# Performance work log

Measured on AMD Instinct MI355X. Metric: run time of the kernel, lower is better.

The kernel has to match this reference:

```python
import jax, jax.numpy as jnp
import numpy as np
from jax import lax

MAX_T = 1.0
MAX_Z = float(np.e)  # exp(MAX_T)
BITS = 8


def weight_quantization(w):
    # tanh -> scale by max-abs (no grad through alpha) -> clamp -> round with STE
    w = jnp.tanh(w)
    alpha = lax.stop_gradient(jnp.max(jnp.abs(w)))
    q = 2 ** (BITS - 1) - 1
    w = jnp.clip(w / alpha, -1.0, 1.0) * q
    w = w + lax.stop_gradient(jnp.round(w) - w)
    return w * alpha / q


def t_linear_c(inp, W, max_spike_time):
    # inp: [B, L, Fin], W: [Fout, Fin] -> out: [B, L, Fout]
    idx = jnp.argsort(inp, axis=-1)                              # [B,L,Fin]
    s_inp = jnp.take_along_axis(inp, idx, axis=-1)[..., None]    # [B,L,Fin,1]
    w_sorted = W.T[idx]                                          # [B,L,Fin,Fout]
    w_sorted = weight_quantization(w_sorted)
    mul = s_inp * w_sorted
    w_sum = jnp.cumsum(w_sorted, axis=-2)
    iw_sum = jnp.cumsum(mul, axis=-2)
    out_all = iw_sum / jnp.clip(w_sum - 1.0, 1e-10, 1e10)
    o = jnp.where(w_sum < 1.0, max_spike_time, out_all)
    o = jnp.where(o < s_inp, max_spike_time, o)
    nxt = jnp.concatenate([s_inp[:, :, 1:, :], jnp.ones_like(s_inp[:, :, :1, :])], axis=2)
    o = jnp.where(o > nxt, max_spike_time, o)
    return jnp.min(o, axis=-2)


def t_linear(inp, W, max_spike_time):
    # inp: [B, Fin], W: [Fout, Fin] -> out: [B, Fout]
    idx = jnp.argsort(inp, axis=-1)
    s_inp = jnp.take_along_axis(inp, idx, axis=-1)[..., None]    # [B,Fin,1]
    w_sorted = W.T[idx]                                          # [B,Fin,Fout]
    mul = s_inp * w_sorted
    w_sum = jnp.cumsum(w_sorted, axis=1)
    iw_sum = jnp.cumsum(mul, axis=1)
    out_all = iw_sum / jnp.clip(w_sum - 1.0, 1e-10, 1e10)
    o = jnp.where(w_sum < 1.0, max_spike_time, out_all)
    o = jnp.where(o < s_inp, max_spike_time, o)
    nxt = jnp.concatenate([s_inp[:, 1:, :], jnp.ones_like(s_inp[:, :1, :])], axis=1)
    o = jnp.where(o >= nxt, max_spike_time, o)  # note: >= in t_Linear (vs > in t_Linear_c)
    return jnp.min(o, axis=1)


def unfold(x, k, p, s):
    # torch F.unfold: zero-pad, extract kxk patches; feature order (C, kh, kw)
    B, C, H, W = x.shape
    xp = jnp.pad(x, ((0, 0), (0, 0), (p, p), (p, p)))
    oh = (H + 2 * p - k) // s + 1
    ow = (W + 2 * p - k) // s + 1
    ri = (jnp.arange(oh) * s)[:, None] + jnp.arange(k)           # [oh,k]
    ci = (jnp.arange(ow) * s)[:, None] + jnp.arange(k)           # [ow,k]
    pt = xp[:, :, ri[:, None, :, None], ci[None, :, None, :]]    # [B,C,oh,ow,k,k]
    pt = pt.transpose(0, 2, 3, 1, 4, 5).reshape(B, oh * ow, C * k * k)
    return pt, oh, ow


def t_conv(x, W, k, pad, stride, max_spike_time):
    B = x.shape[0]
    patches, oh, ow = unfold(x, k, pad, stride)                  # [B,L,C*k*k]
    patches = jnp.where(patches < 0.1, max_spike_time, patches)
    out = t_linear_c(patches, W, max_spike_time)                 # [B,L,Cout]
    return out.transpose(0, 2, 1).reshape(B, W.shape[0], oh, ow)


def max_pool2(x):
    return lax.reduce_window(x, -jnp.inf, lax.max, (1, 1, 2, 2), (1, 1, 2, 2), 'VALID')


def min_pool3(x):
    # -MaxPool3x3(stride 2)(-ConstantPad2d(1, 1e5)(x))
    xp = jnp.pad(x, ((0, 0), (0, 0), (1, 1), (1, 1)), constant_values=1e5)
    return -lax.reduce_window(-xp, -jnp.inf, lax.max, (1, 1, 3, 3), (1, 1, 2, 2), 'VALID')


def setup_inputs() -> dict:
    key = jax.random.key(0)
    ks = jax.random.split(key, 8)
    B = 8
    inp = jax.random.normal(ks[0], (B, 1, 64, 64), dtype=jnp.float32)
    conv1_w = jax.random.normal(ks[1], (32, 1, 5, 5), dtype=jnp.float32) * (1.0 / 5.0)
    bn_g = jnp.ones((32,), jnp.float32)
    bn_b = jnp.zeros((32,), jnp.float32)
    bn_m = jnp.zeros((32,), jnp.float32)
    bn_v = jnp.ones((32,), jnp.float32)
    def uw(k, fout, fin):
        return jax.random.uniform(k, (fout, fin), jnp.float32, 0.0, 10.0 / fin)
    w2 = uw(ks[2], 32, 3 * 3 * 32)
    w3 = uw(ks[3], 32, 3 * 3 * 32)
    w4 = uw(ks[4], 64, 3 * 3 * 32)
    w5 = uw(ks[5], 64, 3 * 3 * 64)
    w_fc = uw(ks[6], 10, 8 * 8 * 64)
    return {"inp": inp, "conv1_w": conv1_w, "bn_g": bn_g, "bn_b": bn_b,
            "bn_m": bn_m, "bn_v": bn_v, "w2": w2, "w3": w3, "w4": w4,
            "w5": w5, "w_fc": w_fc}


def reference(inp, conv1_w, bn_g, bn_b, bn_m, bn_v, w2, w3, w4, w5, w_fc):
    x = lax.conv_general_dilated(inp, conv1_w, (1, 1), ((2, 2), (2, 2)),
                                 dimension_numbers=('NCHW', 'OIHW', 'NCHW'))
    x = (x - bn_m[None, :, None, None]) * (bn_g / jnp.sqrt(bn_v + 1e-5))[None, :, None, None] \
        + bn_b[None, :, None, None]
    x = jax.nn.relu(x)
    x = max_pool2(x)                       # [B,32,32,32]
    x = jnp.minimum(x, MAX_T)
    z1 = jnp.exp(x)
    z2 = t_conv(z1, w2, 3, 1, 2, MAX_Z)    # [B,32,16,16]
    z3 = t_conv(z2, w3, 3, 1, 1, MAX_Z)    # [B,32,16,16]
    z3c = z3 * min_pool3(z1)
    z4 = t_conv(z3c, w4, 3, 1, 2, MAX_Z * 2)  # [B,64,8,8]
    z5 = t_conv(z4, w5, 3, 1, 1, MAX_Z * 2)   # [B,64,8,8]
    pm = min_pool3(z3c)                       # [B,32,8,8]
    pm = jnp.concatenate([pm, pm], axis=1)    # [B,64,8,8]
    z5c = (z5 * pm).reshape(z5.shape[0], -1)  # [B,4096]
    return t_linear(z5c, w_fc, MAX_Z * 4)     # [B,10]
```

## Files before the change

### kernel.cpp

```cpp
#include <hip/hip_runtime.h>
#include <hip/hip_bf16.h>
#include <math.h>

#define E32 2.7182817459106445f

__device__ __forceinline__ unsigned long long packkey(float vf, int idx) {
  unsigned u = __float_as_uint(vf);
  u = (u & 0x80000000u) ? ~u : (u | 0x80000000u);
  return (((unsigned long long)u) << 32) | (unsigned)idx;
}
__device__ __forceinline__ float unpackval(unsigned long long k) {
  unsigned m = (unsigned)(k >> 32);
  m = (m & 0x80000000u) ? (m ^ 0x80000000u) : ~m;
  return __uint_as_float(m);
}

__global__ __launch_bounds__(256) void tanh_max_kernel(
    const float* __restrict__ w2, const float* __restrict__ w3,
    const float* __restrict__ w4, const float* __restrict__ w5,
    float* __restrict__ tanhbuf, float* __restrict__ partials) {
  int blk = blockIdx.x;
  const float* w; int base_blk, tbase;
  if (blk < 36)       { w = w2; base_blk = 0;   tbase = 0; }
  else if (blk < 72)  { w = w3; base_blk = 36;  tbase = 9216; }
  else if (blk < 144) { w = w4; base_blk = 72;  tbase = 18432; }
  else                { w = w5; base_blk = 144; tbase = 36864; }
  int i = (blk - base_blk) * 256 + threadIdx.x;
  float t = tanhf(w[i]);
  tanhbuf[tbase + i] = t;
  __shared__ float red[256];
  red[threadIdx.x] = fabsf(t);
  __syncthreads();
  for (int s = 128; s > 0; s >>= 1) {
    if (threadIdx.x < s) red[threadIdx.x] = fmaxf(red[threadIdx.x], red[threadIdx.x + s]);
    __syncthreads();
  }
  if (threadIdx.x == 0) partials[blk] = red[0];
}

__global__ __launch_bounds__(256) void quantT_kernel(
    const float* __restrict__ tanhbuf, const float* __restrict__ partials,
    float* __restrict__ q2, float* __restrict__ q3,
    float* __restrict__ q4, float* __restrict__ q5,
    const float* __restrict__ wfc, float* __restrict__ wfcT) {
  int blk = blockIdx.x;
  if (blk >= 288) {
    int o = (blk - 288) * 256 + threadIdx.x;
    if (o < 40960) {
      int n = o / 10, f = o % 10;
      wfcT[o] = wfc[f * 4096 + n];
    }
    return;
  }
  float* dst; int base_blk, tbase, pb0, pb1, F, N;
  if (blk < 36)       { dst = q2; base_blk = 0;   tbase = 0;     pb0 = 0;   pb1 = 36;  F = 32; N = 288; }
  else if (blk < 72)  { dst = q3; base_blk = 36;  tbase = 9216;  pb0 = 36;  pb1 = 72;  F = 32; N = 288; }
  else if (blk < 144) { dst = q4; base_blk = 72;  tbase = 18432; pb0 = 72;  pb1 = 144; F = 64; N = 288; }
  else                { dst = q5; base_blk = 144; tbase = 36864; pb0 = 144; pb1 = 288; F = 64; N = 576; }
  __shared__ float red[256];
  float mx = 0.0f;
  for (int j = pb0 + threadIdx.x; j < pb1; j += 256) mx = fmaxf(mx, partials[j]);
  red[threadIdx.x] = mx;
  __syncthreads();
  for (int s = 128; s > 0; s >>= 1) {
    if (threadIdx.x < s) red[threadIdx.x] = fmaxf(red[threadIdx.x], red[threadIdx.x + s]);
    __syncthreads();
  }
  float a = red[0];
  int i = (blk - base_blk) * 256 + threadIdx.x;
  float t = tanhbuf[tbase + i];
  int f = i / N, n = i % N;
  float r = fminf(fmaxf(t / a, -1.0f), 1.0f) * 127.0f;
  dst[n * F + f] = rintf(r) * a / 127.0f;
}

__global__ __launch_bounds__(256) void conv1_kernel(
    const float* __restrict__ inp, const float* __restrict__ w,
    const float* __restrict__ g, const float* __restrict__ bb,
    const float* __restrict__ m, const float* __restrict__ vv,
    float* __restrict__ z1) {
  int idx = blockIdx.x * 256 + threadIdx.x;
  if (idx >= 8 * 32 * 32 * 32) return;
  int x = idx & 31, y = (idx >> 5) & 31, c = (idx >> 10) & 31, b = idx >> 15;
  float scale = g[c] / sqrtf(vv[c] + 1e-5f);
  float bias = bb[c];
  float mean = m[c];
  float mx = -3.402823466e38f;
  for (int dy = 0; dy < 2; ++dy) {
    for (int dx = 0; dx < 2; ++dx) {
      int oy = 2 * y + dy, ox = 2 * x + dx;
      float acc = 0.0f;
      for (int kh = 0; kh < 5; ++kh) {
        int r = oy + kh - 2;
        if (r < 0 || r >= 64) continue;
        for (int kw = 0; kw < 5; ++kw) {
          int cc2 = ox + kw - 2;
          if (cc2 < 0 || cc2 >= 64) continue;
          acc += w[c * 25 + kh * 5 + kw] * inp[(b * 64 + r) * 64 + cc2];
        }
      }
      float xs = (acc - mean) * scale + bias;
      xs = fmaxf(xs, 0.0f);
      mx = fmaxf(mx, xs);
    }
  }
  mx = fminf(mx, 1.0f);
  z1[idx] = (mx == 1.0f) ? E32 : expf(mx);
}

__global__ __launch_bounds__(256) void mp3_kernel(
    const float* __restrict__ in, float* __restrict__ out, int BC, int H) {
  int OH = H >> 1;
  int total = BC * OH * OH;
  int idx = blockIdx.x * 256 + threadIdx.x;
  if (idx >= total) return;
  int j = idx % OH, i = (idx / OH) % OH, bc = idx / (OH * OH);
  float mn = 100000.0f;
  for (int di = 0; di < 3; ++di) {
    int r = 2 * i - 1 + di;
    if (r < 0 || r >= H) continue;
    for (int dj = 0; dj < 3; ++dj) {
      int cc = 2 * j - 1 + dj;
      if (cc < 0 || cc >= H) continue;
      mn = fminf(mn, in[bc * H * H + r * H + cc]);
    }
  }
  out[idx] = mn;
}

__global__ __launch_bounds__(256) void mp3mul_kernel(
    const float* __restrict__ a, const float* __restrict__ b2,
    float* __restrict__ out, int BC, int H) {
  int OH = H >> 1;
  int total = BC * OH * OH;
  int idx = blockIdx.x * 256 + threadIdx.x;
  if (idx >= total) return;
  int j = idx % OH, i = (idx / OH) % OH, bc = idx / (OH * OH);
  float mn = 100000.0f;
  for (int di = 0; di < 3; ++di) {
    int r = 2 * i - 1 + di;
    if (r < 0 || r >= H) continue;
    for (int dj = 0; dj < 3; ++dj) {
      int cc = 2 * j - 1 + dj;
      if (cc < 0 || cc >= H) continue;
      int q = bc * H * H + r * H + cc;
      mn = fminf(mn, __fmul_rn(a[q], b2[q]));
    }
  }
  out[idx] = mn;
}

template <int CIN, int F, int S, int HIN, bool MUL>
__global__ __launch_bounds__(512, 1) void tconv_kernel(
    const float* __restrict__ in, const float* __restrict__ in2,
    const float* __restrict__ wqt, float* __restrict__ out, float MST) {
  constexpr int N = CIN * 9;
  constexpr int NP = (N <= 512) ? 512 : 1024;
  constexpr int KP = NP / 512;
  constexpr int OH = (HIN - 1) / S + 1;
  constexpr int P = OH * OH;
  constexpr int T = 512;
  constexpr int NCH = N / 32;

  __shared__ __align__(16) unsigned long long pk[NP];
  __shared__ float sval[N + 1];
  __shared__ unsigned short sidx[N];
  __shared__ float wbuf[2][32 * F];
  __shared__ float wc[NCH][F];
  __shared__ float iwc[NCH][F];
  __shared__ float pmin[F * NCH];

  int blk = blockIdx.x;
  int b = blk / P, p = blk % P;
  int ph = p / OH, pw = p % OH;
  int tid = threadIdx.x;

  for (int n = tid; n < NP; n += T) {
    if (n < N) {
      int c = n / 9, kk = n % 9, kh = kk / 3, kw = kk % 3;
      int r = ph * S + kh - 1, cc = pw * S + kw - 1;
      float v = 0.0f;
      if (r >= 0 && r < HIN && cc >= 0 && cc < HIN) {
        int q = ((b * CIN + c) * HIN + r) * HIN + cc;
        v = MUL ? __fmul_rn(in[q], in2[q]) : in[q];
      }
      pk[n] = packkey((v < 0.1f) ? MST : v, n);
    } else {
      pk[n] = ~0ull;
    }
  }
  if (tid == 0) sval[N] = 1.0f;
  __syncthreads();

  if constexpr (KP == 1) {
    unsigned long long k0 = pk[tid];
    __syncthreads();
    for (int lk = 1; lk <= 9; ++lk) {
      for (int lj = lk - 1; lj >= 0; --lj) {
        int j = 1 << lj;
        bool up = ((tid >> lk) & 1) == 0;
        bool wmin = (((tid & j) == 0) == up);
        unsigned long long o;
        if (lj >= 6) {
          pk[tid] = k0;
          __syncthreads();
          o = pk[tid ^ j];
          __syncthreads();
        } else {
          o = __shfl_xor(k0, j, 64);
        }
        k0 = wmin ? (k0 < o ? k0 : o) : (k0 > o ? k0 : o);
      }
    }
    if (tid < N) {
      sval[tid] = unpackval(k0);
      sidx[tid] = (unsigned short)(k0 & 0xffffull);
    }
  } else {
    unsigned long long k0 = pk[2 * tid], k1 = pk[2 * tid + 1];
    __syncthreads();
    for (int lk = 1; lk <= 10; ++lk) {
      for (int lj = lk - 1; lj >= 0; --lj) {
        bool up = ((tid >> (lk - 1)) & 1) == 0;
        if (lj == 0) {
          if ((k0 > k1) == up) { unsigned long long t2 = k0; k0 = k1; k1 = t2; }
        } else {
          int tj = 1 << (lj - 1);
          bool wmin = (((tid & tj) == 0) == up);
          unsigned long long o0, o1;
          if (lj >= 7) {
            pk[tid] = k0; pk[512 + tid] = k1;
            __syncthreads();
            o0 = pk[tid ^ tj]; o1 = pk[512 + (tid ^ tj)];
            __syncthreads();
          } else {
            o0 = __shfl_xor(k0, tj, 64);
            o1 = __shfl_xor(k1, tj, 64);
          }
          k0 = wmin ? (k0 < o0 ? k0 : o0) : (k0 > o0 ? k0 : o0);
          k1 = wmin ? (k1 < o1 ? k1 : o1) : (k1 > o1 ? k1 : o1);
        }
      }
    }
    int i0 = tid * 2;
    if (i0 < N) {
      sval[i0] = unpackval(k0);
      sidx[i0] = (unsigned short)(k0 & 0xffffull);
    }
    if (i0 + 1 < N) {
      sval[i0 + 1] = unpackval(k1);
      sidx[i0 + 1] = (unsigned short)(k1 & 0xffffull);
    }
  }
  __syncthreads();

  for (int t = tid; t < 32 * F; t += T) {
    int q = t / F, f = t % F;
    wbuf[0][t] = wqt[(int)sidx[q] * F + f];
  }
  __syncthreads();

  float wsum = 0.0f, iwsum = 0.0f;
  for (int c = 0; c < NCH; ++c) {
    if (tid >= 64 && c + 1 < NCH) {
      int i0n = (c + 1) * 32;
      float* nb = wbuf[(c + 1) & 1];
      for (int t = tid - 64; t < 32 * F; t += (T - 64)) {
        int q = t / F, f = t % F;
        nb[t] = wqt[(int)sidx[i0n + q] * F + f];
      }
    }
    if (tid < F) {
      const float* wb = wbuf[c & 1];
      wc[c][tid] = wsum;
      iwc[c][tid] = iwsum;
      int i0 = c * 32;
#pragma unroll
      for (int q0 = 0; q0 < 32; q0 += 8) {
        float w8[8], s8[8];
#pragma unroll
        for (int r = 0; r < 8; ++r) {
          w8[r] = wb[(q0 + r) * F + tid];
          s8[r] = sval[i0 + q0 + r];
        }
#pragma unroll
        for (int r = 0; r < 8; ++r) {
          wsum = __fadd_rn(wsum, w8[r]);
          iwsum = __fadd_rn(iwsum, __fmul_rn(s8[r], w8[r]));
        }
      }
    }
    __syncthreads();
  }

  for (int task = tid; task < NCH * F; task += T) {
    int c = task / F, f = task % F;
    float ws = wc[c][f], iws = iwc[c][f], omin = 3.402823466e38f;
    int i0 = c * 32;
#pragma unroll
    for (int q0 = 0; q0 < 32; q0 += 8) {
      float wv8[8], sv8[8], nv8[8];
#pragma unroll
      for (int r = 0; r < 8; ++r) {
        int i = i0 + q0 + r;
        wv8[r] = wqt[(int)sidx[i] * F + f];
        sv8[r] = sval[i];
        nv8[r] = sval[i + 1];
      }
#pragma unroll
      for (int r = 0; r < 8; ++r) {
        ws = __fadd_rn(ws, wv8[r]);
        iws = __fadd_rn(iws, __fmul_rn(sv8[r], wv8[r]));
        float den = fminf(fmaxf(__fadd_rn(ws, -1.0f), 1e-10f), 1e10f);
        float oa = iws / den;
        float o = (ws < 1.0f) ? MST : oa;
        o = (o < sv8[r]) ? MST : o;
        o = (o > nv8[r]) ? MST : o;
        omin = fminf(omin, o);
      }
    }
    pmin[f * NCH + c] = omin;
  }
  __syncthreads();

  if (tid < F) {
    float m2 = pmin[tid * NCH];
#pragma unroll
    for (int c = 1; c < NCH; ++c) m2 = fminf(m2, pmin[tid * NCH + c]);
    out[(b * F + tid) * P + p] = m2;
  }
}

#define CE(x, y) { int i_ = (tid << 3) + (x); \
  bool up_ = (((i_ >> lk) & 1) == 0); \
  unsigned long long a_ = k[(x)], c_ = k[(y)]; \
  if ((a_ > c_) == up_) { k[(x)] = c_; k[(y)] = a_; } }

__global__ __launch_bounds__(512, 1) void fc_kernel(
    const float* __restrict__ z5, const float* __restrict__ m3,
    const float* __restrict__ wfcT, float* __restrict__ out) {
  constexpr int NN = 4096;
  __shared__ __align__(16) unsigned long long keys[NN];
  __shared__ __align__(16) float sval[NN + 1];
  __shared__ __align__(16) unsigned short sidx[NN];
  __shared__ float wc[64][10];
  __shared__ float iwc[64][10];
  __shared__ float pmin[64][10];
  float* wsA = (float*)keys;
  float* wsB = (float*)keys + 2608;

  int b = blockIdx.x, tid = threadIdx.x, lane = tid & 63;

  unsigned long long k[8];
  {
    int c = tid >> 3, p0 = (tid << 3) & 63;
    const float4* z4p = (const float4*)(z5 + (b * 64 + c) * 64 + p0);
    const float4* m4p = (const float4*)(m3 + (b * 32 + (c & 31)) * 64 + p0);
    float4 za = z4p[0], zb = z4p[1], ma = m4p[0], mb = m4p[1];
    int n0 = tid << 3;
    k[0] = packkey(__fmul_rn(za.x, ma.x), n0 + 0);
    k[1] = packkey(__fmul_rn(za.y, ma.y), n0 + 1);
    k[2] = packkey(__fmul_rn(za.z, ma.z), n0 + 2);
    k[3] = packkey(__fmul_rn(za.w, ma.w), n0 + 3);
    k[4] = packkey(__fmul_rn(zb.x, mb.x), n0 + 4);
    k[5] = packkey(__fmul_rn(zb.y, mb.y), n0 + 5);
    k[6] = packkey(__fmul_rn(zb.z, mb.z), n0 + 6);
    k[7] = packkey(__fmul_rn(zb.w, mb.w), n0 + 7);
  }

  for (int lk = 1; lk <= 12; ++lk) {
    for (int lj = lk - 1; lj >= 0; --lj) {
      if (lj >= 9) {
        int pm = 1 << (lj - 3);
#pragma unroll
        for (int m = 0; m < 8; ++m) keys[m * 512 + tid] = k[m];
        __syncthreads();
        bool lower = ((tid & pm) == 0);
        bool up = (((tid >> (lk - 3)) & 1) == 0);
        bool wmin = (lower == up);
#pragma unroll
        for (int m = 0; m < 8; ++m) {
          unsigned long long o = keys[m * 512 + (tid ^ pm)];
          unsigned long long mine = k[m];
          k[m] = wmin ? (mine < o ? mine : o) : (mine > o ? mine : o);
        }
        __syncthreads();
      } else if (lj >= 3) {
        int lm = 1 << (lj - 3);
        bool lower = ((lane & lm) == 0);
        bool up = (((tid >> (lk - 3)) & 1) == 0);
        bool wmin = (lower == up);
#pragma unroll
        for (int m = 0; m < 8; ++m) {
          unsigned long long o = __shfl_xor(k[m], lm, 64);
          unsigned long long mine = k[m];
          k[m] = wmin ? (mine < o ? mine : o) : (mine > o ? mine : o);
        }
      } else if (lj == 2) {
        CE(0, 4) CE(1, 5) CE(2, 6) CE(3, 7)
      } else if (lj == 1) {
        CE(0, 2) CE(1, 3) CE(4, 6) CE(5, 7)
      } else {
        CE(0, 1) CE(2, 3) CE(4, 5) CE(6, 7)
      }
    }
  }

  {
    float4 v0, v1;
    v0.x = unpackval(k[0]); v0.y = unpackval(k[1]);
    v0.z = unpackval(k[2]); v0.w = unpackval(k[3]);
    v1.x = unpackval(k[4]); v1.y = unpackval(k[5]);
    v1.z = unpackval(k[6]); v1.w = unpackval(k[7]);
    ((float4*)sval)[tid * 2] = v0;
    ((float4*)sval)[tid * 2 + 1] = v1;
    ushort si[8];
#pragma unroll
    for (int m = 0; m < 8; ++m) si[m] = (unsigned short)(k[m] & 0xffffull);
    ((ulong2*)sidx)[tid] = *(ulong2*)si;
  }
  if (tid == 0) sval[NN] = 1.0f;
  __syncthreads();

  {
    float tmp[5];
#pragma unroll
    for (int u = 0; u < 5; ++u) {
      int t = tid + u * 512;
      tmp[u] = wfcT[(int)sidx[t / 10] * 10 + (t % 10)];
    }
#pragma unroll
    for (int u = 0; u < 5; ++u) {
      int t = tid + u * 512;
      wsA[(t % 10) * 260 + t / 10] = tmp[u];
    }
  }
  __syncthreads();

  float wsum = 0.0f, iwsum = 0.0f;
  for (int c = 0; c < 16; ++c) {
    int c0 = c * 256;
    float* cur = (c & 1) ? wsB : wsA;
    float* nxt = (c & 1) ? wsA : wsB;
    if (tid >= 64 && c + 1 < 16) {
      int c0n = c0 + 256;
      float tmp[6];
#pragma unroll
      for (int u = 0; u < 6; ++u) {
        int t = (tid - 64) + u * 448;
        tmp[u] = (t < 2560) ? wfcT[(int)sidx[c0n + t / 10] * 10 + (t % 10)] : 0.0f;
      }
#pragma unroll
      for (int u = 0; u < 6; ++u) {
        int t = (tid - 64) + u * 448;
        if (t < 2560) nxt[(t % 10) * 260 + t / 10] = tmp[u];
      }
    }
    if (tid < 10) {
      const float* wrow = cur + tid * 260;
      float4 wA4[4], sA4[4], wB4[4], sB4[4];
      auto LD = [&](int i0, float4* w4, float4* s4) {
#pragma unroll
        for (int kq = 0; kq < 4; ++kq) {
          w4[kq] = *(const float4*)(wrow + i0 + 4 * kq);
          s4[kq] = *(const float4*)(sval + c0 + i0 + 4 * kq);
        }
      };
      auto ACC = [&](const float4* w4, const float4* s4) {
#pragma unroll
        for (int kq = 0; kq < 4; ++kq) {
          float w0 = w4[kq].x, w1 = w4[kq].y, w2 = w4[kq].z, w3 = w4[kq].w;
          float s0 = s4[kq].x, s1 = s4[kq].y, s2 = s4[kq].z, s3 = s4[kq].w;
          wsum = __fadd_rn(wsum, w0); iwsum = __fadd_rn(iwsum, __fmul_rn(s0, w0));
          wsum = __fadd_rn(wsum, w1); iwsum = __fadd_rn(iwsum, __fmul_rn(s1, w1));
          wsum = __fadd_rn(wsum, w2); iwsum = __fadd_rn(iwsum, __fmul_rn(s2, w2));
          wsum = __fadd_rn(wsum, w3); iwsum = __fadd_rn(iwsum, __fmul_rn(s3, w3));
        }
      };
      LD(0, wA4, sA4);
      for (int i0 = 0; i0 < 256; i0 += 32) {
        if ((i0 & 63) == 0) {
          int cc = (c0 + i0) >> 6;
          wc[cc][tid] = wsum;
          iwc[cc][tid] = iwsum;
        }
        LD(i0 + 16, wB4, sB4);
        ACC(wA4, sA4);
        if (i0 + 32 < 256) LD(i0 + 32, wA4, sA4);
        ACC(wB4, sB4);
      }
    }
    __syncthreads();
  }

  const float MST = 4.0f * E32;
  for (int task = tid; task < 640; task += 512) {
    int c = task / 10, f = task % 10;
    float wsr = wc[c][f], iwsr = iwc[c][f], omin = 3.402823466e38f;
    int i0 = c * 64;
    for (int q0 = 0; q0 < 64; q0 += 8) {
      float wv8[8], sv8[8], nv8[8];
#pragma unroll
      for (int r = 0; r < 8; ++r) {
        int i = i0 + q0 + r;
        wv8[r] = wfcT[(int)sidx[i] * 10 + f];
        sv8[r] = sval[i];
        nv8[r] = sval[i + 1];
      }
#pragma unroll
      for (int r = 0; r < 8; ++r) {
        wsr = __fadd_rn(wsr, wv8[r]);
        iwsr = __fadd_rn(iwsr, __fmul_rn(sv8[r], wv8[r]));
        float den = fminf(fmaxf(__fadd_rn(wsr, -1.0f), 1e-10f), 1e10f);
        float oa = iwsr / den;
        float o = (wsr < 1.0f) ? MST : oa;
        o = (o < sv8[r]) ? MST : o;
        o = (o >= nv8[r]) ? MST : o;
        omin = fminf(omin, o);
      }
    }
    pmin[c][f] = omin;
  }
  __syncthreads();

  if (tid < 10) {
    float m = pmin[0][tid];
#pragma unroll
    for (int c = 1; c < 64; ++c) m = fminf(m, pmin[c][tid]);
    out[b * 10 + tid] = m;
  }
}
#undef CE

extern "C" void kernel_launch(void* const* d_in, const int* in_sizes, int n_in,
                              void* d_out, int out_size, void* d_ws, size_t ws_size,
                              hipStream_t stream) {
  const float* inp   = (const float*)d_in[0];
  const float* w1    = (const float*)d_in[1];
  const float* bn_g  = (const float*)d_in[2];
  const float* bn_b  = (const float*)d_in[3];
  const float* bn_m  = (const float*)d_in[4];
  const float* bn_v  = (const float*)d_in[5];
  const float* w2    = (const float*)d_in[6];
  const float* w3    = (const float*)d_in[7];
  const float* w4    = (const float*)d_in[8];
  const float* w5    = (const float*)d_in[9];
  const float* wfc   = (const float*)d_in[10];
  float* out = (float*)d_out;

  float* ws = (float*)d_ws;
  float* wq2 = ws + 16;
  float* wq3 = wq2 + 9216;
  float* wq4 = wq3 + 9216;
  float* wq5 = wq4 + 18432;
  float* z1  = wq5 + 36864;
  float* m1  = z1 + 262144;
  float* z2  = m1 + 65536;
  float* z3  = z2 + 65536;
  float* m3  = z3 + 65536;
  float* z4  = m3 + 16384;
  float* z5  = z4 + 32768;
  float* tanhbuf  = z5 + 32768;
  float* partials = tanhbuf + 73728;
  float* wfcT = partials + 512;

  tanh_max_kernel<<<288, 256, 0, stream>>>(w2, w3, w4, w5, tanhbuf, partials);
  quantT_kernel<<<448, 256, 0, stream>>>(tanhbuf, partials, wq2, wq3, wq4, wq5, wfc, wfcT);

  conv1_kernel<<<1024, 256, 0, stream>>>(inp, w1, bn_g, bn_b, bn_m, bn_v, z1);
  mp3_kernel<<<256, 256, 0, stream>>>(z1, m1, 8 * 32, 32);

  tconv_kernel<32, 32, 2, 32, false><<<8 * 256, 512, 0, stream>>>(z1, nullptr, wq2, z2, E32);
  tconv_kernel<32, 32, 1, 16, false><<<8 * 256, 512, 0, stream>>>(z2, nullptr, wq3, z3, E32);
  mp3mul_kernel<<<64, 256, 0, stream>>>(z3, m1, m3, 8 * 32, 16);
  tconv_kernel<32, 64, 2, 16, true><<<8 * 64, 512, 0, stream>>>(z3, m1, wq4, z4, 2.0f * E32);
  tconv_kernel<64, 64, 1, 8, false><<<8 * 64, 512, 0, stream>>>(z4, nullptr, wq5, z5, 2.0f * E32);

  fc_kernel<<<8, 512, 0, stream>>>(z5, m3, wfcT, out);
}
```

Measured before the change: 255.3 us.

## Split FC stage into sort kernel and per-(batch,output) scan kernel

The fused FC kernel is split into a bitonic sort kernel that writes sorted values and indices to workspace, and a scan kernel launched with 80 blocks, one per batch/output pair, instead of 8 blocks. The sort loops are also unrolled at compile time through recursive templates, so pass parameters become constants. The serial prefix scan per output now runs in its own block over 4096 elements with a single thread, in place of the earlier double-buffered 10-thread scheme, and the later segment pass uses 128 threads. The cost is an extra launch, a global round trip for the sorted data, and a long single-thread serial scan per block.

Result: no change. 251.1 us (-1.7%).

```diff
diff --git a/kernel.cpp b/kernel.cpp
--- a/kernel.cpp
+++ b/kernel.cpp
@@ -331,24 +331,70 @@
   }
 }
 
-#define CE(x, y) { int i_ = (tid << 3) + (x); \
-  bool up_ = (((i_ >> lk) & 1) == 0); \
-  unsigned long long a_ = k[(x)], c_ = k[(y)]; \
-  if ((a_ > c_) == up_) { k[(x)] = c_; k[(y)] = a_; } }
-
-__global__ __launch_bounds__(512, 1) void fc_kernel(
+template <int LK, int LJ>
+__device__ __forceinline__ void bpass(unsigned long long (&k)[8],
+                                      unsigned long long* keys,
+                                      int tid, int lane) {
+  if constexpr (LJ >= 9) {
+    constexpr int pm = 1 << (LJ - 3);
+#pragma unroll
+    for (int m = 0; m < 8; ++m) keys[m * 512 + tid] = k[m];
+    __syncthreads();
+    bool lower = ((tid & pm) == 0);
+    bool up = (((tid >> (LK - 3)) & 1) == 0);
+    bool wmin = (lower == up);
+#pragma unroll
+    for (int m = 0; m < 8; ++m) {
+      unsigned long long o = keys[m * 512 + (tid ^ pm)];
+      unsigned long long mine = k[m];
+      k[m] = wmin ? (mine < o ? mine : o) : (mine > o ? mine : o);
+    }
+    __syncthreads();
+  } else if constexpr (LJ >= 3) {
+    constexpr int lm = 1 << (LJ - 3);
+    bool lower = ((lane & lm) == 0);
+    bool up = (((tid >> (LK - 3)) & 1) == 0);
+    bool wmin = (lower == up);
+#pragma unroll
+    for (int m = 0; m < 8; ++m) {
+      unsigned long long o = __shfl_xor(k[m], lm, 64);
+      unsigned long long mine = k[m];
+      k[m] = wmin ? (mine < o ? mine : o) : (mine > o ? mine : o);
+    }
+  } else {
+    constexpr int j = 1 << LJ;
+#pragma unroll
+    for (int m = 0; m < 8; ++m) {
+      if ((m & j) == 0) {
+        int i = (tid << 3) + m;
+        bool up = (((i >> LK) & 1) == 0);
+        unsigned long long a = k[m], c2 = k[m | j];
+        if ((a > c2) == up) { k[m] = c2; k[m | j] = a; }
+      }
+    }
+  }
+}
+
+template <int LK, int LJ>
+__device__ __forceinline__ void bpasses(unsigned long long (&k)[8],
+                                        unsigned long long* keys,
+                                        int tid, int lane) {
+  bpass<LK, LJ>(k, keys, tid, lane);
+  if constexpr (LJ > 0) bpasses<LK, LJ - 1>(k, keys, tid, lane);
+}
+
+template <int LK>
+__device__ __forceinline__ void bstages(unsigned long long (&k)[8],
+                                        unsigned long long* keys,
+                                        int tid, int lane) {
+  bpasses<LK, LK - 1>(k, keys, tid, lane);
+  if constexpr (LK < 12) bstages<LK + 1>(k, keys, tid, lane);
+}
+
+__global__ __launch_bounds__(512, 1) void fc_sort_kernel(
     const float* __restrict__ z5, const float* __restrict__ m3,
-    const float* __restrict__ wfcT, float* __restrict__ out) {
-  constexpr int NN = 4096;
-  __shared__ __align__(16) unsigned long long keys[NN];
-  __shared__ __align__(16) float sval[NN + 1];
-  __shared__ __align__(16) unsigned short sidx[NN];
-  __shared__ float wc[64][10];
-  __shared__ float iwc[64][10];
-  __shared__ float pmin[64][10];
-  float* wsA = (float*)keys;
-  float* wsB = (float*)keys + 2608;
-
+    float* __restrict__ svalG, unsigned short* __restrict__ sidxG) {
+  __shared__ __align__(16) unsigned long long keys[4096];
   int b = blockIdx.x, tid = threadIdx.x, lane = tid & 63;
 
   unsigned long long k[8];
@@ -368,43 +414,7 @@
     k[7] = packkey(__fmul_rn(zb.w, mb.w), n0 + 7);
   }
 
-  for (int lk = 1; lk <= 12; ++lk) {
-    for (int lj = lk - 1; lj >= 0; --lj) {
-      if (lj >= 9) {
-        int pm = 1 << (lj - 3);
-#pragma unroll
-        for (int m = 0; m < 8; ++m) keys[m * 512 + tid] = k[m];
-        __syncthreads();
-        bool lower = ((tid & pm) == 0);
-        bool up = (((tid >> (lk - 3)) & 1) == 0);
-        bool wmin = (lower == up);
-#pragma unroll
-        for (int m = 0; m < 8; ++m) {
-          unsigned long long o = keys[m * 512 + (tid ^ pm)];
-          unsigned long long mine = k[m];
-          k[m] = wmin ? (mine < o ? mine : o) : (mine > o ? mine : o);
-        }
-        __syncthreads();
-      } else if (lj >= 3) {
-        int lm = 1 << (lj - 3);
-        bool lower = ((lane & lm) == 0);
-        bool up = (((tid >> (lk - 3)) & 1) == 0);
-        bool wmin = (lower == up);
-#pragma unroll
-        for (int m = 0; m < 8; ++m) {
-          unsigned long long o = __shfl_xor(k[m], lm, 64);
-          unsigned long long mine = k[m];
-          k[m] = wmin ? (mine < o ? mine : o) : (mine > o ? mine : o);
-        }
-      } else if (lj == 2) {
-        CE(0, 4) CE(1, 5) CE(2, 6) CE(3, 7)
-      } else if (lj == 1) {
-        CE(0, 2) CE(1, 3) CE(4, 6) CE(5, 7)
-      } else {
-        CE(0, 1) CE(2, 3) CE(4, 5) CE(6, 7)
-      }
-    }
-  }
+  bstages<1>(k, keys, tid, lane);
 
   {
     float4 v0, v1;
@@ -412,125 +422,118 @@
     v0.z = unpackval(k[2]); v0.w = unpackval(k[3]);
     v1.x = unpackval(k[4]); v1.y = unpackval(k[5]);
     v1.z = unpackval(k[6]); v1.w = unpackval(k[7]);
-    ((float4*)sval)[tid * 2] = v0;
-    ((float4*)sval)[tid * 2 + 1] = v1;
+    float* svalRow = svalG + b * 4104;
+    ((float4*)svalRow)[tid * 2] = v0;
+    ((float4*)svalRow)[tid * 2 + 1] = v1;
     ushort si[8];
 #pragma unroll
     for (int m = 0; m < 8; ++m) si[m] = (unsigned short)(k[m] & 0xffffull);
-    ((ulong2*)sidx)[tid] = *(ulong2*)si;
-  }
-  if (tid == 0) sval[NN] = 1.0f;
+    ((ulong2*)(sidxG + b * 4096))[tid] = *(ulong2*)si;
+    if (tid == 0) svalRow[4096] = 1.0f;
+  }
+}
+
+__global__ __launch_bounds__(512, 1) void fc_scan2_kernel(
+    const float* __restrict__ svalG, const unsigned short* __restrict__ sidxG,
+    const float* __restrict__ wfcT, float* __restrict__ out) {
+  constexpr int NN = 4096;
+  __shared__ __align__(16) float sval[NN + 1];
+  __shared__ __align__(16) unsigned short sidx[NN];
+  __shared__ __align__(16) float wlds[NN];
+  __shared__ float wc[128], iwc[128];
+  __shared__ float pmin[128];
+
+  int blk = blockIdx.x;
+  int b = blk / 10, f = blk % 10;
+  int tid = threadIdx.x;
+  const float* svalRow = svalG + b * 4104;
+
+  for (int t = tid; t < 1024; t += 512)
+    ((float4*)sval)[t] = ((const float4*)svalRow)[t];
+  ((ulong2*)sidx)[tid] = ((const ulong2*)(sidxG + b * 4096))[tid];
+  if (tid == 0) sval[NN] = svalRow[4096];
   __syncthreads();
 
   {
-    float tmp[5];
-#pragma unroll
-    for (int u = 0; u < 5; ++u) {
-      int t = tid + u * 512;
-      tmp[u] = wfcT[(int)sidx[t / 10] * 10 + (t % 10)];
-    }
-#pragma unroll
-    for (int u = 0; u < 5; ++u) {
-      int t = tid + u * 512;
-      wsA[(t % 10) * 260 + t / 10] = tmp[u];
-    }
-  }
-  __syncthreads();
-
-  float wsum = 0.0f, iwsum = 0.0f;
-  for (int c = 0; c < 16; ++c) {
-    int c0 = c * 256;
-    float* cur = (c & 1) ? wsB : wsA;
-    float* nxt = (c & 1) ? wsA : wsB;
-    if (tid >= 64 && c + 1 < 16) {
-      int c0n = c0 + 256;
-      float tmp[6];
-#pragma unroll
-      for (int u = 0; u < 6; ++u) {
-        int t = (tid - 64) + u * 448;
-        tmp[u] = (t < 2560) ? wfcT[(int)sidx[c0n + t / 10] * 10 + (t % 10)] : 0.0f;
-      }
-#pragma unroll
-      for (int u = 0; u < 6; ++u) {
-        int t = (tid - 64) + u * 448;
-        if (t < 2560) nxt[(t % 10) * 260 + t / 10] = tmp[u];
-      }
-    }
-    if (tid < 10) {
-      const float* wrow = cur + tid * 260;
-      float4 wA4[4], sA4[4], wB4[4], sB4[4];
-      auto LD = [&](int i0, float4* w4, float4* s4) {
-#pragma unroll
-        for (int kq = 0; kq < 4; ++kq) {
-          w4[kq] = *(const float4*)(wrow + i0 + 4 * kq);
-          s4[kq] = *(const float4*)(sval + c0 + i0 + 4 * kq);
-        }
-      };
-      auto ACC = [&](const float4* w4, const float4* s4) {
-#pragma unroll
-        for (int kq = 0; kq < 4; ++kq) {
-          float w0 = w4[kq].x, w1 = w4[kq].y, w2 = w4[kq].z, w3 = w4[kq].w;
-          float s0 = s4[kq].x, s1 = s4[kq].y, s2 = s4[kq].z, s3 = s4[kq].w;
-          wsum = __fadd_rn(wsum, w0); iwsum = __fadd_rn(iwsum, __fmul_rn(s0, w0));
-          wsum = __fadd_rn(wsum, w1); iwsum = __fadd_rn(iwsum, __fmul_rn(s1, w1));
-          wsum = __fadd_rn(wsum, w2); iwsum = __fadd_rn(iwsum, __fmul_rn(s2, w2));
-          wsum = __fadd_rn(wsum, w3); iwsum = __fadd_rn(iwsum, __fmul_rn(s3, w3));
-        }
-      };
-      LD(0, wA4, sA4);
-      for (int i0 = 0; i0 < 256; i0 += 32) {
-        if ((i0 & 63) == 0) {
-          int cc = (c0 + i0) >> 6;
-          wc[cc][tid] = wsum;
-          iwc[cc][tid] = iwsum;
-        }
-        LD(i0 + 16, wB4, sB4);
-        ACC(wA4, sA4);
-        if (i0 + 32 < 256) LD(i0 + 32, wA4, sA4);
-        ACC(wB4, sB4);
-      }
-    }
-    __syncthreads();
-  }
+    int idx8[8];
+    float tmp[8];
+#pragma unroll
+    for (int u = 0; u < 8; ++u) idx8[u] = sidx[tid + u * 512];
+#pragma unroll
+    for (int u = 0; u < 8; ++u) tmp[u] = wfcT[idx8[u] * 10 + f];
+#pragma unroll
+    for (int u = 0; u < 8; ++u) wlds[tid + u * 512] = tmp[u];
+  }
+  __syncthreads();
+
+  if (tid == 0) {
+    float wsum = 0.0f, iwsum = 0.0f;
+    float4 wA4[4], sA4[4], wB4[4], sB4[4];
+    auto LD = [&](int i0, float4* w4, float4* s4) {
+#pragma unroll
+      for (int kq = 0; kq < 4; ++kq) {
+        w4[kq] = *(const float4*)(wlds + i0 + 4 * kq);
+        s4[kq] = *(const float4*)(sval + i0 + 4 * kq);
+      }
+    };
+    auto ACC = [&](const float4* w4, const float4* s4) {
+#pragma unroll
+      for (int kq = 0; kq < 4; ++kq) {
+        float w0 = w4[kq].x, w1 = w4[kq].y, w2 = w4[kq].z, w3 = w4[kq].w;
+        float s0 = s4[kq].x, s1 = s4[kq].y, s2 = s4[kq].z, s3 = s4[kq].w;
+        wsum = __fadd_rn(wsum, w0); iwsum = __fadd_rn(iwsum, __fmul_rn(s0, w0));
+        wsum = __fadd_rn(wsum, w1); iwsum = __fadd_rn(iwsum, __fmul_rn(s1, w1));
+        wsum = __fadd_rn(wsum, w2); iwsum = __fadd_rn(iwsum, __fmul_rn(s2, w2));
+        wsum = __fadd_rn(wsum, w3); iwsum = __fadd_rn(iwsum, __fmul_rn(s3, w3));
+      }
+    };
+    LD(0, wA4, sA4);
+    for (int i0 = 0; i0 < NN; i0 += 32) {
+      wc[i0 >> 5] = wsum;
+      iwc[i0 >> 5] = iwsum;
+      LD(i0 + 16, wB4, sB4);
+      ACC(wA4, sA4);
+      if (i0 + 32 < NN) LD(i0 + 32, wA4, sA4);
+      ACC(wB4, sB4);
+    }
+  }
+  __syncthreads();
 
   const float MST = 4.0f * E32;
-  for (int task = tid; task < 640; task += 512) {
-    int c = task / 10, f = task % 10;
-    float wsr = wc[c][f], iwsr = iwc[c][f], omin = 3.402823466e38f;
-    int i0 = c * 64;
-    for (int q0 = 0; q0 < 64; q0 += 8) {
+  if (tid < 128) {
+    float ws = wc[tid], iws = iwc[tid], omin = 3.402823466e38f;
+    int i0 = tid * 32;
+    for (int q0 = 0; q0 < 32; q0 += 8) {
       float wv8[8], sv8[8], nv8[8];
 #pragma unroll
       for (int r = 0; r < 8; ++r) {
         int i = i0 + q0 + r;
-        wv8[r] = wfcT[(int)sidx[i] * 10 + f];
+        wv8[r] = wlds[i];
         sv8[r] = sval[i];
         nv8[r] = sval[i + 1];
       }
 #pragma unroll
       for (int r = 0; r < 8; ++r) {
-        wsr = __fadd_rn(wsr, wv8[r]);
-        iwsr = __fadd_rn(iwsr, __fmul_rn(sv8[r], wv8[r]));
-        float den = fminf(fmaxf(__fadd_rn(wsr, -1.0f), 1e-10f), 1e10f);
-        float oa = iwsr / den;
-        float o = (wsr < 1.0f) ? MST : oa;
+        ws = __fadd_rn(ws, wv8[r]);
+        iws = __fadd_rn(iws, __fmul_rn(sv8[r], wv8[r]));
+        float den = fminf(fmaxf(__fadd_rn(ws, -1.0f), 1e-10f), 1e10f);
+        float oa = iws / den;
+        float o = (ws < 1.0f) ? MST : oa;
         o = (o < sv8[r]) ? MST : o;
         o = (o >= nv8[r]) ? MST : o;
         omin = fminf(omin, o);
       }
     }
-    pmin[c][f] = omin;
-  }
-  __syncthreads();
-
-  if (tid < 10) {
-    float m = pmin[0][tid];
-#pragma unroll
-    for (int c = 1; c < 64; ++c) m = fminf(m, pmin[c][tid]);
-    out[b * 10 + tid] = m;
-  }
-}
-#undef CE
+    pmin[tid] = omin;
+  }
+  __syncthreads();
+
+  if (tid == 0) {
+    float m = pmin[0];
+    for (int c = 1; c < 128; ++c) m = fminf(m, pmin[c]);
+    out[b * 10 + f] = m;
+  }
+}
 
 extern "C" void kernel_launch(void* const* d_in, const int* in_sizes, int n_in,
                               void* d_out, int out_size, void* d_ws, size_t ws_size,
@@ -563,6 +566,8 @@
   float* tanhbuf  = z5 + 32768;
   float* partials = tanhbuf + 73728;
   float* wfcT = partials + 512;
+  float* svalG = wfcT + 40960;
+  unsigned short* sidxG = (unsigned short*)(svalG + 32832);
 
   tanh_max_kernel<<<288, 256, 0, stream>>>(w2, w3, w4, w5, tanhbuf, partials);
   quantT_kernel<<<448, 256, 0, stream>>>(tanhbuf, partials, wq2, wq3, wq4, wq5, wfc, wfcT);
@@ -576,5 +581,6 @@
   tconv_kernel<32, 64, 2, 16, true><<<8 * 64, 512, 0, stream>>>(z3, m1, wq4, z4, 2.0f * E32);
   tconv_kernel<64, 64, 1, 8, false><<<8 * 64, 512, 0, stream>>>(z4, nullptr, wq5, z5, 2.0f * E32);
 
-  fc_kernel<<<8, 512, 0, stream>>>(z5, m3, wfcT, out);
-}
+  fc_sort_kernel<<<8, 512, 0, stream>>>(z5, m3, svalG, sidxG);
+  fc_scan2_kernel<<<80, 512, 0, stream>>>(svalG, sidxG, wfcT, out);
+}
```
